# Kernel tuning notes

Hardware: AMD Instinct MI355X
Metric: run time of the kernel (lower is better)

Reference implementation:

```python
import jax, jax.numpy as jnp
import numpy as np

B, N, M = 16, 4096, 4096

def setup_inputs() -> dict:
    key = jax.random.key(0)
    k1, k2, k3 = jax.random.split(key, 3)
    src_points = jax.random.normal(k1, (B, N, 3), dtype=jnp.float32)
    tgt_points = jax.random.normal(k2, (B, M, 3), dtype=jnp.float32)
    weights = jax.random.uniform(k3, (B,), dtype=jnp.float32)
    return {"src_points": src_points, "tgt_points": tgt_points, "weights": weights}

def reference(src_points, tgt_points, weights):
    # Pairwise squared distances per batch: [B, N, M]
    # ||s - t||^2 = ||s||^2 + ||t||^2 - 2 s.t  (single dense intermediate)
    s2 = jnp.sum(src_points * src_points, axis=-1)  # [B, N]
    t2 = jnp.sum(tgt_points * tgt_points, axis=-1)  # [B, M]
    cross = jnp.einsum('bnd,bmd->bnm', src_points, tgt_points)  # [B, N, M]
    d2 = s2[:, :, None] + t2[:, None, :] - 2.0 * cross          # [B, N, M]
    d2 = jnp.maximum(d2, 0.0)  # numerical guard
    # Bidirectional chamfer: mean of nearest-neighbor squared distances
    d_src_to_tgt = jnp.mean(jnp.min(d2, axis=2), axis=1)  # [B]
    d_tgt_to_src = jnp.mean(jnp.min(d2, axis=1), axis=1)  # [B]
    distances = d_src_to_tgt + d_tgt_to_src               # [B]
    distances = distances * weights
    return jnp.mean(distances)  # reduction='mean'
```

## Files before the change

### kernel.cpp

```cpp
#include <hip/hip_runtime.h>

#define BQ 16
#define NP 4096
#define MP 4096

constexpr int TPB = 256;
constexpr int WAVES = 4;
constexpr int FR = 2;
constexpr int COLS_PER_BLOCK = 32 * FR * WAVES;
constexpr int ROWSPLIT = 2;
constexpr int GROUPS_PER_BLOCK = (MP / 32) / ROWSPLIT;

typedef __bf16 bf16x8 __attribute__((ext_vector_type(8)));
typedef float f32x16 __attribute__((ext_vector_type(16)));

union Frag {
    unsigned short u[8];
    bf16x8 v;
    int4 i4;
};

__device__ inline unsigned short f2bf(float f) {
    unsigned u = __float_as_uint(f);
    return (unsigned short)((u + 0x7FFFu + ((u >> 16) & 1u)) >> 16);
}
__device__ inline float bf2f(unsigned short h) {
    return __uint_as_float(((unsigned)h) << 16);
}

__global__ __launch_bounds__(TPB) void chamfer_prep_kernel(
    const float* __restrict__ srcp, const float* __restrict__ tgtp,
    unsigned short* __restrict__ table, unsigned int* __restrict__ minbuf,
    float* __restrict__ out) {
    const int idx = blockIdx.x * TPB + threadIdx.x;
    const int gy  = idx >> 12;
    const int t   = idx & 4095;
    const int dir = gy >> 4, b = gy & 15;
    const float* rows = dir ? (srcp + (size_t)b * NP * 3)
                            : (tgtp + (size_t)b * MP * 3);
    const float* p = rows + (size_t)t * 3;
    float x = p[0], y = p[1], z = p[2];
    unsigned short xh = f2bf(x), yh = f2bf(y), zh = f2bf(z);
    unsigned short xl = f2bf(x - bf2f(xh));
    unsigned short yl = f2bf(y - bf2f(yh));
    unsigned short zl = f2bf(z - bf2f(zh));
    float t2 = fmaf(x, x, fmaf(y, y, z * z));
    unsigned short t2h = f2bf(t2), t2l = f2bf(t2 - bf2f(t2h));
    const unsigned short ONE = 0x3F80;
    Frag p0, p1;
    p0.u[0] = xh; p0.u[1] = yh; p0.u[2] = zh;
    p0.u[3] = xh; p0.u[4] = yh; p0.u[5] = zh;
    p0.u[6] = xl; p0.u[7] = yl;
    p1.u[0] = zl;
    p1.u[1] = t2h; p1.u[2] = t2l;
    p1.u[3] = ONE; p1.u[4] = ONE;
    p1.u[5] = 0; p1.u[6] = 0; p1.u[7] = 0;
    unsigned short* dst = table + ((size_t)gy << 16) + ((t >> 5) << 9) + ((t & 31) << 4);
    *(int4*)(dst)     = p0.i4;
    *(int4*)(dst + 8) = p1.i4;
    minbuf[idx] = 0x7F800000u;
    if (idx == 0) out[0] = 0.0f;
}

__global__ __launch_bounds__(TPB) void chamfer_main_kernel(
    const float* __restrict__ srcp, const float* __restrict__ tgtp,
    const unsigned short* __restrict__ table,
    unsigned int* __restrict__ minbuf) {
    const int gy  = blockIdx.z;
    const int dir = gy >> 4;
    const int b   = gy & 15;
    const float* S = dir ? (tgtp + (size_t)b * MP * 3) : (srcp + (size_t)b * NP * 3);
    unsigned int* mb = minbuf + ((size_t)gy << 12);

    const int tid  = threadIdx.x;
    const int lane = tid & 63;
    const int half = lane >> 5;
    const int col  = lane & 31;
    const int wave = tid >> 6;

    const unsigned short ONE = 0x3F80;

    Frag bfr[FR];
#pragma unroll
    for (int f = 0; f < FR; ++f) {
        const int sidx = blockIdx.x * COLS_PER_BLOCK + (wave * FR + f) * 32 + col;
        const float* sp = S + (size_t)sidx * 3;
        float x = sp[0], y = sp[1], z = sp[2];
        unsigned short uh0 = f2bf(-2.0f * x), uh1 = f2bf(-2.0f * y), uh2 = f2bf(-2.0f * z);
        unsigned short ul0 = f2bf(-2.0f * x - bf2f(uh0));
        unsigned short ul1 = f2bf(-2.0f * y - bf2f(uh1));
        unsigned short ul2 = f2bf(-2.0f * z - bf2f(uh2));
        float s2 = fmaf(x, x, fmaf(y, y, z * z));
        unsigned short s2h = f2bf(s2), s2l = f2bf(s2 - bf2f(s2h));
        if (half == 0) {
            bfr[f].u[0] = uh0; bfr[f].u[1] = uh1; bfr[f].u[2] = uh2;
            bfr[f].u[3] = ul0; bfr[f].u[4] = ul1; bfr[f].u[5] = ul2;
            bfr[f].u[6] = uh0; bfr[f].u[7] = uh1;
        } else {
            bfr[f].u[0] = uh2; bfr[f].u[1] = ONE; bfr[f].u[2] = ONE;
            bfr[f].u[3] = s2h; bfr[f].u[4] = s2l;
            bfr[f].u[5] = 0;   bfr[f].u[6] = 0;  bfr[f].u[7] = 0;
        }
    }

    float accm[FR];
#pragma unroll
    for (int f = 0; f < FR; ++f) accm[f] = __int_as_float(0x7F800000);

    const f32x16 zc = {};

    const unsigned short* lptr = table + ((size_t)gy << 16) +
                                 ((size_t)blockIdx.y * GROUPS_PER_BLOCK << 9) +
                                 (col << 4) + (half << 3);

#pragma unroll 4
    for (int g = 0; g < GROUPS_PER_BLOCK; ++g) {
        Frag a;
        a.i4 = *(const int4*)(lptr + ((size_t)g << 9));
#pragma unroll
        for (int f = 0; f < FR; ++f) {
            f32x16 d = __builtin_amdgcn_mfma_f32_32x32x16_bf16(a.v, bfr[f].v, zc, 0, 0, 0);
            float m0 = fminf(fminf(d[0], d[1]), d[2]);
            float m1 = fminf(fminf(d[3], d[4]), d[5]);
            float m2 = fminf(fminf(d[6], d[7]), d[8]);
            float m3 = fminf(fminf(d[9], d[10]), d[11]);
            float m4 = fminf(fminf(d[12], d[13]), d[14]);
            float t0 = fminf(fminf(m0, m1), m2);
            float t1 = fminf(fminf(m3, m4), d[15]);
            accm[f] = fminf(fminf(accm[f], t0), t1);
        }
    }

#pragma unroll
    for (int f = 0; f < FR; ++f) {
        float m = fminf(accm[f], __shfl_xor(accm[f], 32, 64));
        m = fmaxf(m, 0.0f);
        if (lane < 32) {
            const int sidx = blockIdx.x * COLS_PER_BLOCK + (wave * FR + f) * 32 + col;
            atomicMin(&mb[sidx], __float_as_uint(m));
        }
    }
}

__global__ __launch_bounds__(TPB) void chamfer_reduce_kernel(
    const float* __restrict__ minbuf, const float* __restrict__ weights,
    float* __restrict__ out) {
    const int idx = blockIdx.x;
    const int b = idx & 15;
    const float* m0 = minbuf + ((size_t)idx << 12);

    float s = 0.0f;
    for (int i = threadIdx.x; i < 4096; i += TPB) s += m0[i];
#pragma unroll
    for (int off = 32; off > 0; off >>= 1) s += __shfl_down(s, off, 64);

    __shared__ float red[TPB / 64];
    if ((threadIdx.x & 63) == 0) red[threadIdx.x >> 6] = s;
    __syncthreads();
    if (threadIdx.x == 0) {
        float tot = red[0] + red[1] + red[2] + red[3];
        atomicAdd(out, weights[b] * tot * (1.0f / (4096.0f * (float)BQ)));
    }
}

__global__ void chamfer_zero_kernel(float* __restrict__ out) { out[0] = 0.0f; }

__global__ __launch_bounds__(TPB) void chamfer_fb_kernel(
    const float* __restrict__ srcp, const float* __restrict__ tgtp,
    const float* __restrict__ wts, float* __restrict__ out) {
    const int gy = blockIdx.y, dir = gy >> 4, b = gy & 15;
    const float* S = dir ? (tgtp + (size_t)b * MP * 3) : (srcp + (size_t)b * NP * 3);
    const float* T = dir ? (srcp + (size_t)b * NP * 3) : (tgtp + (size_t)b * MP * 3);
    const int tid = threadIdx.x, lane = tid & 63, half = lane >> 5,
              col = lane & 31, wave = tid >> 6;
    __shared__ unsigned short sh[256 * 16];
    __shared__ float partial[WAVES];
    const unsigned short ONE = 0x3F80;
    Frag bfr[FR];
#pragma unroll
    for (int f = 0; f < FR; ++f) {
        const int sidx = blockIdx.x * COLS_PER_BLOCK + (wave * FR + f) * 32 + col;
        const float* sp = S + (size_t)sidx * 3;
        float x = sp[0], y = sp[1], z = sp[2];
        unsigned short uh0 = f2bf(-2.0f * x), uh1 = f2bf(-2.0f * y), uh2 = f2bf(-2.0f * z);
        unsigned short ul0 = f2bf(-2.0f * x - bf2f(uh0));
        unsigned short ul1 = f2bf(-2.0f * y - bf2f(uh1));
        unsigned short ul2 = f2bf(-2.0f * z - bf2f(uh2));
        float s2 = fmaf(x, x, fmaf(y, y, z * z));
        unsigned short s2h = f2bf(s2), s2l = f2bf(s2 - bf2f(s2h));
        if (half == 0) {
            bfr[f].u[0] = uh0; bfr[f].u[1] = uh1; bfr[f].u[2] = uh2;
            bfr[f].u[3] = ul0; bfr[f].u[4] = ul1; bfr[f].u[5] = ul2;
            bfr[f].u[6] = uh0; bfr[f].u[7] = uh1;
        } else {
            bfr[f].u[0] = uh2; bfr[f].u[1] = ONE; bfr[f].u[2] = ONE;
            bfr[f].u[3] = s2h; bfr[f].u[4] = s2l;
            bfr[f].u[5] = 0;   bfr[f].u[6] = 0;  bfr[f].u[7] = 0;
        }
    }
    float accm[FR];
#pragma unroll
    for (int f = 0; f < FR; ++f) accm[f] = __int_as_float(0x7F800000);
    const f32x16 zc = {};
    const int sub = tid >> 5, row = tid & 31;
    float cx, cy, cz;
    { const float* tp = T + (size_t)tid * 3; cx = tp[0]; cy = tp[1]; cz = tp[2]; }
    for (int c = 0; c < MP / 256; ++c) {
        {
            unsigned short xh = f2bf(cx), yh = f2bf(cy), zh = f2bf(cz);
            unsigned short xl = f2bf(cx - bf2f(xh));
            unsigned short yl = f2bf(cy - bf2f(yh));
            unsigned short zl = f2bf(cz - bf2f(zh));
            float t2 = fmaf(cx, cx, fmaf(cy, cy, cz * cz));
            unsigned short t2h = f2bf(t2), t2l = f2bf(t2 - bf2f(t2h));
            Frag p0, p1;
            p0.u[0] = xh; p0.u[1] = yh; p0.u[2] = zh;
            p0.u[3] = xh; p0.u[4] = yh; p0.u[5] = zh;
            p0.u[6] = xl; p0.u[7] = yl;
            p1.u[0] = zl; p1.u[1] = t2h; p1.u[2] = t2l;
            p1.u[3] = ONE; p1.u[4] = ONE; p1.u[5] = 0; p1.u[6] = 0; p1.u[7] = 0;
            *(int4*)&sh[((sub * 2 + 0) * 32 + row) * 8] = p0.i4;
            *(int4*)&sh[((sub * 2 + 1) * 32 + row) * 8] = p1.i4;
        }
        __syncthreads();
        if (c + 1 < MP / 256) {
            const float* tp = T + (size_t)((c + 1) * 256 + tid) * 3;
            cx = tp[0]; cy = tp[1]; cz = tp[2];
        }
#pragma unroll
        for (int sc = 0; sc < 8; ++sc) {
            Frag a;
            a.i4 = *(const int4*)&sh[((sc * 2 + half) * 32 + col) * 8];
#pragma unroll
            for (int f = 0; f < FR; ++f) {
                f32x16 d = __builtin_amdgcn_mfma_f32_32x32x16_bf16(a.v, bfr[f].v, zc, 0, 0, 0);
                float m0 = fminf(fminf(d[0], d[1]), d[2]);
                float m1 = fminf(fminf(d[3], d[4]), d[5]);
                float m2 = fminf(fminf(d[6], d[7]), d[8]);
                float m3 = fminf(fminf(d[9], d[10]), d[11]);
                float m4 = fminf(fminf(d[12], d[13]), d[14]);
                accm[f] = fminf(accm[f], fminf(fminf(fminf(m0, m1), m2),
                                               fminf(fminf(m3, m4), d[15])));
            }
        }
        __syncthreads();
    }
    float tot = 0.0f;
#pragma unroll
    for (int f = 0; f < FR; ++f) {
        float m = fminf(accm[f], __shfl_xor(accm[f], 32, 64));
        tot += fmaxf(m, 0.0f);
    }
#pragma unroll
    for (int off = 32; off > 0; off >>= 1) tot += __shfl_xor(tot, off, 64);
    if (lane == 0) partial[wave] = tot * 0.5f;
    __syncthreads();
    if (tid == 0) {
        float v = partial[0] + partial[1] + partial[2] + partial[3];
        atomicAdd(out, v * wts[b] * (1.0f / ((float)NP * (float)BQ)));
    }
}

extern "C" void kernel_launch(void* const* d_in, const int* in_sizes, int n_in,
                              void* d_out, int out_size, void* d_ws, size_t ws_size,
                              hipStream_t stream) {
    const float* src = (const float*)d_in[0];
    const float* tgt = (const float*)d_in[1];
    const float* wts = (const float*)d_in[2];
    float* out = (float*)d_out;

    const size_t MINBUF_BYTES = (size_t)2 * BQ * 4096 * 4;
    const size_t TABLE_BYTES  = (size_t)2 * BQ * 4096 * 32;

    if (ws_size >= MINBUF_BYTES + TABLE_BYTES) {
        unsigned int* minbuf  = (unsigned int*)d_ws;
        unsigned short* table = (unsigned short*)((char*)d_ws + MINBUF_BYTES);

        chamfer_prep_kernel<<<(2 * BQ * 4096) / TPB, TPB, 0, stream>>>(
            src, tgt, table, minbuf, out);

        dim3 grid(NP / COLS_PER_BLOCK, ROWSPLIT, 2 * BQ);
        chamfer_main_kernel<<<grid, TPB, 0, stream>>>(src, tgt, table, minbuf);

        chamfer_reduce_kernel<<<2 * BQ, TPB, 0, stream>>>(
            (const float*)minbuf, wts, out);
    } else {
        chamfer_zero_kernel<<<1, 1, 0, stream>>>(out);
        dim3 grid(NP / COLS_PER_BLOCK, 2 * BQ);
        chamfer_fb_kernel<<<grid, TPB, 0, stream>>>(src, tgt, wts, out);
    }
}
```

Before: 99.36 us.

## Switch main kernel to 16x16x32 MFMA with LDS-staged point table chunks

The main kernel now uses 16x16x32 bf16 MFMA instead of 32x32x16. Each wave handles 4 fragments of 16 columns, and the point table is laid out linearly and staged through shared memory in 512-row chunks, with a zero pad for the unused K lanes. The aim is to cut the per-MFMA min-reduction cost (4 outputs instead of 16 per lane) and to make table reads coalesced and reused across waves. In exchange it adds block-wide barriers with no double buffering, and half of each MFMA's K dimension is zero padding.

```diff
diff --git a/kernel.cpp b/kernel.cpp
--- a/kernel.cpp
+++ b/kernel.cpp
@@ -6,13 +6,14 @@
 
 constexpr int TPB = 256;
 constexpr int WAVES = 4;
-constexpr int FR = 2;
-constexpr int COLS_PER_BLOCK = 32 * FR * WAVES;
+constexpr int FR = 4;
+constexpr int COLS_PER_BLOCK = 16 * FR * WAVES;
 constexpr int ROWSPLIT = 2;
-constexpr int GROUPS_PER_BLOCK = (MP / 32) / ROWSPLIT;
+constexpr int ROWS_PER_BLOCK = MP / ROWSPLIT;
+constexpr int CHUNK = 512;
 
 typedef __bf16 bf16x8 __attribute__((ext_vector_type(8)));
-typedef float f32x16 __attribute__((ext_vector_type(16)));
+typedef float f32x4 __attribute__((ext_vector_type(4)));
 
 union Frag {
     unsigned short u[8];
@@ -48,14 +49,11 @@
     unsigned short t2h = f2bf(t2), t2l = f2bf(t2 - bf2f(t2h));
     const unsigned short ONE = 0x3F80;
     Frag p0, p1;
-    p0.u[0] = xh; p0.u[1] = yh; p0.u[2] = zh;
-    p0.u[3] = xh; p0.u[4] = yh; p0.u[5] = zh;
-    p0.u[6] = xl; p0.u[7] = yl;
-    p1.u[0] = zl;
-    p1.u[1] = t2h; p1.u[2] = t2l;
-    p1.u[3] = ONE; p1.u[4] = ONE;
-    p1.u[5] = 0; p1.u[6] = 0; p1.u[7] = 0;
-    unsigned short* dst = table + ((size_t)gy << 16) + ((t >> 5) << 9) + ((t & 31) << 4);
+    p0.u[0] = xh; p0.u[1] = yh; p0.u[2] = zh; p0.u[3] = xh;
+    p0.u[4] = yh; p0.u[5] = zh; p0.u[6] = xl; p0.u[7] = yl;
+    p1.u[0] = zl; p1.u[1] = t2h; p1.u[2] = t2l; p1.u[3] = ONE;
+    p1.u[4] = ONE; p1.u[5] = 0; p1.u[6] = 0; p1.u[7] = 0;
+    unsigned short* dst = table + ((size_t)gy << 16) + ((size_t)t << 4);
     *(int4*)(dst)     = p0.i4;
     *(int4*)(dst + 8) = p1.i4;
     minbuf[idx] = 0x7F800000u;
@@ -74,16 +72,133 @@
 
     const int tid  = threadIdx.x;
     const int lane = tid & 63;
-    const int half = lane >> 5;
-    const int col  = lane & 31;
+    const int q    = lane >> 4;
+    const int r16  = lane & 15;
     const int wave = tid >> 6;
 
+    __shared__ unsigned short sh[CHUNK * 16 + 8];
+
     const unsigned short ONE = 0x3F80;
 
     Frag bfr[FR];
 #pragma unroll
     for (int f = 0; f < FR; ++f) {
-        const int sidx = blockIdx.x * COLS_PER_BLOCK + (wave * FR + f) * 32 + col;
+        const int sidx = blockIdx.x * COLS_PER_BLOCK + wave * (16 * FR) + f * 16 + r16;
+        const float* sp = S + (size_t)sidx * 3;
+        float x = sp[0], y = sp[1], z = sp[2];
+        unsigned short uh0 = f2bf(-2.0f * x), uh1 = f2bf(-2.0f * y), uh2 = f2bf(-2.0f * z);
+        unsigned short ul0 = f2bf(-2.0f * x - bf2f(uh0));
+        unsigned short ul1 = f2bf(-2.0f * y - bf2f(uh1));
+        unsigned short ul2 = f2bf(-2.0f * z - bf2f(uh2));
+        float s2 = fmaf(x, x, fmaf(y, y, z * z));
+        unsigned short s2h = f2bf(s2), s2l = f2bf(s2 - bf2f(s2h));
+        if (q == 0) {
+            bfr[f].u[0] = uh0; bfr[f].u[1] = uh1; bfr[f].u[2] = uh2; bfr[f].u[3] = ul0;
+            bfr[f].u[4] = ul1; bfr[f].u[5] = ul2; bfr[f].u[6] = uh0; bfr[f].u[7] = uh1;
+        } else if (q == 1) {
+            bfr[f].u[0] = uh2; bfr[f].u[1] = ONE; bfr[f].u[2] = ONE; bfr[f].u[3] = s2h;
+            bfr[f].u[4] = s2l; bfr[f].u[5] = 0;  bfr[f].u[6] = 0;  bfr[f].u[7] = 0;
+        } else {
+#pragma unroll
+            for (int j = 0; j < 8; ++j) bfr[f].u[j] = 0;
+        }
+    }
+
+    float accm[FR];
+#pragma unroll
+    for (int f = 0; f < FR; ++f) accm[f] = __int_as_float(0x7F800000);
+
+    const f32x4 zc = {};
+
+    const int aoff  = (q < 2) ? (r16 * 16 + q * 8) : (CHUNK * 16);
+    const int astep = (q < 2) ? 256 : 0;
+
+    const unsigned short* slice =
+        table + ((size_t)gy << 16) + ((size_t)blockIdx.y * ROWS_PER_BLOCK << 4);
+
+    if (tid == 0) {
+        int4 z4 = {0, 0, 0, 0};
+        *(int4*)&sh[CHUNK * 16] = z4;
+    }
+
+    for (int c = 0; c < ROWS_PER_BLOCK / CHUNK; ++c) {
+        {
+            const int4* gp = (const int4*)(slice + ((size_t)c * CHUNK << 4));
+            int4* sp4 = (int4*)sh;
+#pragma unroll
+            for (int k = 0; k < 4; ++k) sp4[tid + k * 256] = gp[tid + k * 256];
+        }
+        __syncthreads();
+
+        const unsigned short* ap = sh + aoff;
+#pragma unroll 4
+        for (int g = 0; g < CHUNK / 16; ++g) {
+            Frag a;
+            a.i4 = *(const int4*)(ap);
+            ap += astep;
+#pragma unroll
+            for (int f = 0; f < FR; ++f) {
+                f32x4 d = __builtin_amdgcn_mfma_f32_16x16x32_bf16(a.v, bfr[f].v, zc, 0, 0, 0);
+                accm[f] = fminf(accm[f],
+                                fminf(fminf(d[0], d[1]), fminf(d[2], d[3])));
+            }
+        }
+        __syncthreads();
+    }
+
+#pragma unroll
+    for (int f = 0; f < FR; ++f) {
+        float m = accm[f];
+        m = fminf(m, __shfl_xor(m, 16, 64));
+        m = fminf(m, __shfl_xor(m, 32, 64));
+        m = fmaxf(m, 0.0f);
+        if (lane < 16) {
+            const int sidx = blockIdx.x * COLS_PER_BLOCK + wave * (16 * FR) + f * 16 + r16;
+            atomicMin(&mb[sidx], __float_as_uint(m));
+        }
+    }
+}
+
+__global__ __launch_bounds__(TPB) void chamfer_reduce_kernel(
+    const float* __restrict__ minbuf, const float* __restrict__ weights,
+    float* __restrict__ out) {
+    const int idx = blockIdx.x;
+    const int b = idx & 15;
+    const float* m0 = minbuf + ((size_t)idx << 12);
+
+    float s = 0.0f;
+    for (int i = threadIdx.x; i < 4096; i += TPB) s += m0[i];
+#pragma unroll
+    for (int off = 32; off > 0; off >>= 1) s += __shfl_down(s, off, 64);
+
+    __shared__ float red[TPB / 64];
+    if ((threadIdx.x & 63) == 0) red[threadIdx.x >> 6] = s;
+    __syncthreads();
+    if (threadIdx.x == 0) {
+        float tot = red[0] + red[1] + red[2] + red[3];
+        atomicAdd(out, weights[b] * tot * (1.0f / (4096.0f * (float)BQ)));
+    }
+}
+
+__global__ void chamfer_zero_kernel(float* __restrict__ out) { out[0] = 0.0f; }
+
+typedef float f32x16 __attribute__((ext_vector_type(16)));
+
+__global__ __launch_bounds__(TPB) void chamfer_fb_kernel(
+    const float* __restrict__ srcp, const float* __restrict__ tgtp,
+    const float* __restrict__ wts, float* __restrict__ out) {
+    const int gy = blockIdx.y, dir = gy >> 4, b = gy & 15;
+    const float* S = dir ? (tgtp + (size_t)b * MP * 3) : (srcp + (size_t)b * NP * 3);
+    const float* T = dir ? (srcp + (size_t)b * NP * 3) : (tgtp + (size_t)b * MP * 3);
+    const int tid = threadIdx.x, lane = tid & 63, half = lane >> 5,
+              col = lane & 31, wave = tid >> 6;
+    __shared__ unsigned short sh[256 * 16];
+    __shared__ float partial[WAVES];
+    const unsigned short ONE = 0x3F80;
+    Frag bfr[2];
+#pragma unroll
+    for (int f = 0; f < 2; ++f) {
+        const int sidx = blockIdx.x * 256 + (wave * 2 + f) * 32 + col;
         const float* sp = S + (size_t)sidx * 3;
         float x = sp[0], y = sp[1], z = sp[2];
         unsigned short uh0 = f2bf(-2.0f * x), uh1 = f2bf(-2.0f * y), uh2 = f2bf(-2.0f * z);
@@ -102,105 +217,7 @@
             bfr[f].u[5] = 0;   bfr[f].u[6] = 0;  bfr[f].u[7] = 0;
         }
     }
-
-    float accm[FR];
-#pragma unroll
-    for (int f = 0; f < FR; ++f) accm[f] = __int_as_float(0x7F800000);
-
-    const f32x16 zc = {};
-
-    const unsigned short* lptr = table + ((size_t)gy << 16) +
-                                 ((size_t)blockIdx.y * GROUPS_PER_BLOCK << 9) +
-                                 (col << 4) + (half << 3);
-
-#pragma unroll 4
-    for (int g = 0; g < GROUPS_PER_BLOCK; ++g) {
-        Frag a;
-        a.i4 = *(const int4*)(lptr + ((size_t)g << 9));
-#pragma unroll
-        for (int f = 0; f < FR; ++f) {
-            f32x16 d = __builtin_amdgcn_mfma_f32_32x32x16_bf16(a.v, bfr[f].v, zc, 0, 0, 0);
-            float m0 = fminf(fminf(d[0], d[1]), d[2]);
-            float m1 = fminf(fminf(d[3], d[4]), d[5]);
-            float m2 = fminf(fminf(d[6], d[7]), d[8]);
-            float m3 = fminf(fminf(d[9], d[10]), d[11]);
-            float m4 = fminf(fminf(d[12], d[13]), d[14]);
-            float t0 = fminf(fminf(m0, m1), m2);
-            float t1 = fminf(fminf(m3, m4), d[15]);
-            accm[f] = fminf(fminf(accm[f], t0), t1);
-        }
-    }
-
-#pragma unroll
-    for (int f = 0; f < FR; ++f) {
-        float m = fminf(accm[f], __shfl_xor(accm[f], 32, 64));
-        m = fmaxf(m, 0.0f);
-        if (lane < 32) {
-            const int sidx = blockIdx.x * COLS_PER_BLOCK + (wave * FR + f) * 32 + col;
-            atomicMin(&mb[sidx], __float_as_uint(m));
-        }
-    }
-}
-
-__global__ __launch_bounds__(TPB) void chamfer_reduce_kernel(
-    const float* __restrict__ minbuf, const float* __restrict__ weights,
-    float* __restrict__ out) {
-    const int idx = blockIdx.x;
-    const int b = idx & 15;
-    const float* m0 = minbuf + ((size_t)idx << 12);
-
-    float s = 0.0f;
-    for (int i = threadIdx.x; i < 4096; i += TPB) s += m0[i];
-#pragma unroll
-    for (int off = 32; off > 0; off >>= 1) s += __shfl_down(s, off, 64);
-
-    __shared__ float red[TPB / 64];
-    if ((threadIdx.x & 63) == 0) red[threadIdx.x >> 6] = s;
-    __syncthreads();
-    if (threadIdx.x == 0) {
-        float tot = red[0] + red[1] + red[2] + red[3];
-        atomicAdd(out, weights[b] * tot * (1.0f / (4096.0f * (float)BQ)));
-    }
-}
-
-__global__ void chamfer_zero_kernel(float* __restrict__ out) { out[0] = 0.0f; }
-
-__global__ __launch_bounds__(TPB) void chamfer_fb_kernel(
-    const float* __restrict__ srcp, const float* __restrict__ tgtp,
-    const float* __restrict__ wts, float* __restrict__ out) {
-    const int gy = blockIdx.y, dir = gy >> 4, b = gy & 15;
-    const float* S = dir ? (tgtp + (size_t)b * MP * 3) : (srcp + (size_t)b * NP * 3);
-    const float* T = dir ? (srcp + (size_t)b * NP * 3) : (tgtp + (size_t)b * MP * 3);
-    const int tid = threadIdx.x, lane = tid & 63, half = lane >> 5,
-              col = lane & 31, wave = tid >> 6;
-    __shared__ unsigned short sh[256 * 16];
-    __shared__ float partial[WAVES];
-    const unsigned short ONE = 0x3F80;
-    Frag bfr[FR];
-#pragma unroll
-    for (int f = 0; f < FR; ++f) {
-        const int sidx = blockIdx.x * COLS_PER_BLOCK + (wave * FR + f) * 32 + col;
-        const float* sp = S + (size_t)sidx * 3;
-        float x = sp[0], y = sp[1], z = sp[2];
-        unsigned short uh0 = f2bf(-2.0f * x), uh1 = f2bf(-2.0f * y), uh2 = f2bf(-2.0f * z);
-        unsigned short ul0 = f2bf(-2.0f * x - bf2f(uh0));
-        unsigned short ul1 = f2bf(-2.0f * y - bf2f(uh1));
-        unsigned short ul2 = f2bf(-2.0f * z - bf2f(uh2));
-        float s2 = fmaf(x, x, fmaf(y, y, z * z));
-        unsigned short s2h = f2bf(s2), s2l = f2bf(s2 - bf2f(s2h));
-        if (half == 0) {
-            bfr[f].u[0] = uh0; bfr[f].u[1] = uh1; bfr[f].u[2] = uh2;
-            bfr[f].u[3] = ul0; bfr[f].u[4] = ul1; bfr[f].u[5] = ul2;
-            bfr[f].u[6] = uh0; bfr[f].u[7] = uh1;
-        } else {
-            bfr[f].u[0] = uh2; bfr[f].u[1] = ONE; bfr[f].u[2] = ONE;
-            bfr[f].u[3] = s2h; bfr[f].u[4] = s2l;
-            bfr[f].u[5] = 0;   bfr[f].u[6] = 0;  bfr[f].u[7] = 0;
-        }
-    }
-    float accm[FR];
-#pragma unroll
-    for (int f = 0; f < FR; ++f) accm[f] = __int_as_float(0x7F800000);
+    float accm[2] = {__int_as_float(0x7F800000), __int_as_float(0x7F800000)};
     const f32x16 zc = {};
     const int sub = tid >> 5, row = tid & 31;
     float cx, cy, cz;
@@ -232,7 +249,7 @@
             Frag a;
             a.i4 = *(const int4*)&sh[((sc * 2 + half) * 32 + col) * 8];
 #pragma unroll
-            for (int f = 0; f < FR; ++f) {
+            for (int f = 0; f < 2; ++f) {
                 f32x16 d = __builtin_amdgcn_mfma_f32_32x32x16_bf16(a.v, bfr[f].v, zc, 0, 0, 0);
                 float m0 = fminf(fminf(d[0], d[1]), d[2]);
                 float m1 = fminf(fminf(d[3], d[4]), d[5]);
@@ -247,7 +264,7 @@
     }
     float tot = 0.0f;
 #pragma unroll
-    for (int f = 0; f < FR; ++f) {
+    for (int f = 0; f < 2; ++f) {
         float m = fminf(accm[f], __shfl_xor(accm[f], 32, 64));
         tot += fmaxf(m, 0.0f);
     }
@@ -286,7 +303,7 @@
             (const float*)minbuf, wts, out);
     } else {
         chamfer_zero_kernel<<<1, 1, 0, stream>>>(out);
-        dim3 grid(NP / COLS_PER_BLOCK, 2 * BQ);
+        dim3 grid(NP / 256, 2 * BQ);
         chamfer_fb_kernel<<<grid, TPB, 0, stream>>>(src, tgt, wts, out);
     }
 }
```

After: 109.6 us. +10.3%, slower.
